# Performance work log

Measured on AMD Instinct MI355X. Metric: run time of the kernel, lower is better.

Reference implementation:

```python
import jax, jax.numpy as jnp
import numpy as np

B, C, H, W, K = 8, 128, 256, 256, 19


def setup_inputs() -> dict:
    key = jax.random.key(0)
    k1, k2, k3, k4, k5, k6 = jax.random.split(key, 6)
    s = 1.0 / np.sqrt(C)
    return {
        "x": jax.random.normal(k1, (B, C, H, W), dtype=jnp.float32),
        "preds": jax.random.normal(k2, (B, K, H, W), dtype=jnp.float32),
        "w1": jax.random.normal(k3, (C, C), dtype=jnp.float32) * s,
        "b1": jax.random.normal(k4, (C,), dtype=jnp.float32) * 0.01,
        "w2": jax.random.normal(k5, (C, C), dtype=jnp.float32) * s,
        "b2": jax.random.normal(k6, (C,), dtype=jnp.float32) * 0.01,
    }


def reference(x, preds, w1, b1, w2, b2):
    b, c, h, w = x.shape
    k = preds.shape[1]
    n = h * w
    xf = x.reshape(b, c, n)          # [B,C,N]
    pf = preds.reshape(b, k, n)      # [B,K,N]

    # --- GCG: argmax-grouped softmax-weighted segment sum, scatter back ---
    cls = jnp.argmax(pf, axis=1)                       # [B,N] per-pixel class
    m = jax.nn.one_hot(cls, k, axis=1, dtype=bool)     # [B,K,N] class membership
    scores = jnp.where(m, pf, -jnp.inf)                # mask logits per class group
    mx = jnp.max(scores, axis=2, keepdims=True)
    mx = jnp.where(jnp.isfinite(mx), mx, 0.0)          # guard empty classes
    e = jnp.where(m, jnp.exp(scores - mx), 0.0)
    wgt = e / jnp.maximum(e.sum(axis=2, keepdims=True), 1e-30)  # [B,K,N] segment softmax
    class_feats = jnp.einsum('bkn,bcn->bkc', wgt, xf)  # [B,K,C] weighted segment sum
    fs = jnp.take_along_axis(class_feats, cls[:, :, None], axis=1)  # [B,N,C] scatter-broadcast

    # --- 1x1 convs + global class attention ---
    x1 = jnp.einsum('bcn,dc->bdn', xf, w1) + b1[None, :, None]  # conv1 -> [B,C,N]
    fs2 = jnp.einsum('bnc,dc->bnd', fs, w2) + b2                # conv2 -> [B,N,C]
    gc = jnp.einsum('bcn,bnd->bcd', x1, fs2) * (c ** -0.5)      # [B,C,C]
    return jax.nn.softmax(gc, axis=-1)
```

## Files before the change

### kernel.cpp

```cpp
#include <hip/hip_runtime.h>

#define K_CLS 19
#define C_CH  128
#define NPIX  65536
#define BATCH 8
#define ROWSTRIDE 39


__global__ __launch_bounds__(256, 2)
void gcg_pass1(const float* __restrict__ preds, unsigned* __restrict__ meta,
               float* __restrict__ deng, float* __restrict__ cntg)
{
    __shared__ float denl[K_CLS], cntl[K_CLS];
    const int t = threadIdx.x;
    const int b = blockIdx.x >> 6, blk = blockIdx.x & 63;
    if (t < K_CLS) { denl[t] = 0.f; cntl[t] = 0.f; }
    __syncthreads();

    const int n0 = blk * 1024 + 4 * t;
    const float* pb = preds + (size_t)b * K_CLS * NPIX + n0;

    float4 bv = *reinterpret_cast<const float4*>(pb);
    int k0 = 0, k1 = 0, k2 = 0, k3 = 0;
    #pragma unroll
    for (int k = 1; k < K_CLS; ++k) {
        const float4 p = *reinterpret_cast<const float4*>(pb + (size_t)k * NPIX);
        if (p.x > bv.x) { bv.x = p.x; k0 = k; }
        if (p.y > bv.y) { bv.y = p.y; k1 = k; }
        if (p.z > bv.z) { bv.z = p.z; k2 = k; }
        if (p.w > bv.w) { bv.w = p.w; k3 = k; }
    }
    uint4 m;
    m.x = (__float_as_uint(__expf(bv.x)) & 0xFFFFFFE0u) | (unsigned)k0;
    m.y = (__float_as_uint(__expf(bv.y)) & 0xFFFFFFE0u) | (unsigned)k1;
    m.z = (__float_as_uint(__expf(bv.z)) & 0xFFFFFFE0u) | (unsigned)k2;
    m.w = (__float_as_uint(__expf(bv.w)) & 0xFFFFFFE0u) | (unsigned)k3;
    *reinterpret_cast<uint4*>(meta + (size_t)b * NPIX + n0) = m;

    atomicAdd(&denl[k0], __uint_as_float(m.x & 0xFFFFFFE0u)); atomicAdd(&cntl[k0], 1.f);
    atomicAdd(&denl[k1], __uint_as_float(m.y & 0xFFFFFFE0u)); atomicAdd(&cntl[k1], 1.f);
    atomicAdd(&denl[k2], __uint_as_float(m.z & 0xFFFFFFE0u)); atomicAdd(&cntl[k2], 1.f);
    atomicAdd(&denl[k3], __uint_as_float(m.w & 0xFFFFFFE0u)); atomicAdd(&cntl[k3], 1.f);
    __syncthreads();
    if (t < K_CLS) {
        unsafeAtomicAdd(&deng[b * K_CLS + t], denl[t]);
        unsafeAtomicAdd(&cntg[b * K_CLS + t], cntl[t]);
    }
}

__global__ __launch_bounds__(256, 4)
void gcg_pass2(const float* __restrict__ x, const unsigned* __restrict__ meta,
               float* __restrict__ WXg, float* __restrict__ SXg)
{
    __shared__ float acc[256 * ROWSTRIDE];
    const int t = threadIdx.x, w = t >> 6, l = t & 63;
    const int b = blockIdx.x >> 7;
    const int r = blockIdx.x & 127;
    const int cgrp = r >> 2, q = r & 3;
    const int c = cgrp * 4 + w;

    float* arow = &acc[t * ROWSTRIDE];
    #pragma unroll
    for (int s = 0; s < ROWSTRIDE; ++s) arow[s] = 0.f;

    const float*    xr = x    + ((size_t)(b * C_CH + c)) * NPIX + q * 16384;
    const unsigned* mr = meta + (size_t)b * NPIX + q * 16384;

    #pragma unroll 4
    for (int i = 0; i < 64; ++i) {
        const int px = i * 256 + 4 * l;
        const float4 x4 = *reinterpret_cast<const float4*>(xr + px);
        const uint4  m4 = *reinterpret_cast<const uint4*>(mr + px);
        {   const int k = (int)(m4.x & 31u);
            const float e = __uint_as_float(m4.x & 0xFFFFFFE0u);
            const float vW = arow[k], vS = arow[19 + k];
            arow[k] = fmaf(e, x4.x, vW); arow[19 + k] = vS + x4.x;
        }
        {   const int k = (int)(m4.y & 31u);
            const float e = __uint_as_float(m4.y & 0xFFFFFFE0u);
            const float vW = arow[k], vS = arow[19 + k];
            arow[k] = fmaf(e, x4.y, vW); arow[19 + k] = vS + x4.y;
        }
        {   const int k = (int)(m4.z & 31u);
            const float e = __uint_as_float(m4.z & 0xFFFFFFE0u);
            const float vW = arow[k], vS = arow[19 + k];
            arow[k] = fmaf(e, x4.z, vW); arow[19 + k] = vS + x4.z;
        }
        {   const int k = (int)(m4.w & 31u);
            const float e = __uint_as_float(m4.w & 0xFFFFFFE0u);
            const float vW = arow[k], vS = arow[19 + k];
            arow[k] = fmaf(e, x4.w, vW); arow[19 + k] = vS + x4.w;
        }
    }
    __syncthreads();

    if (t < 2 * 4 * K_CLS) {
        const int arr = t / (4 * K_CLS), rem = t % (4 * K_CLS);
        const int ww = rem / K_CLS, k = rem % K_CLS;
        const int slot = arr * K_CLS + k;
        float s0 = 0.f;
        #pragma unroll 8
        for (int ll = 0; ll < 64; ++ll)
            s0 += acc[(ww * 64 + ll) * ROWSTRIDE + slot];
        const int cc = cgrp * 4 + ww;
        float* dst = (arr == 0) ? WXg : SXg;
        unsafeAtomicAdd(&dst[((size_t)b * K_CLS + k) * C_CH + cc], s0);
    }
}

__global__ __launch_bounds__(256, 1)
void gcg_epiA(const float* __restrict__ WXg, const float* __restrict__ SXg,
              const float* __restrict__ deng, const float* __restrict__ cntg,
              const float* __restrict__ w1, const float* __restrict__ b1,
              const float* __restrict__ w2,
              float* __restrict__ cf2g, float* __restrict__ S1g)
{
    __shared__ float wb[C_CH * 129];
    __shared__ float fb[K_CLS * 129];
    const int t = threadIdx.x, b = blockIdx.x;

    for (int f = t; f < C_CH * C_CH / 4; f += 256) {
        const int d = f >> 5, c4 = (f & 31) << 2;
        const float4 v = *reinterpret_cast<const float4*>(w2 + d * C_CH + c4);
        float* p = &wb[d * 129 + c4];
        p[0] = v.x; p[1] = v.y; p[2] = v.z; p[3] = v.w;
    }
    for (int i = t; i < K_CLS * C_CH; i += 256) {
        const int k = i >> 7, c = i & 127;
        fb[k * 129 + c] = WXg[(size_t)b * K_CLS * C_CH + i] /
                          fmaxf(deng[b * K_CLS + k], 1e-30f);
    }
    __syncthreads();
    for (int i = t; i < K_CLS * C_CH; i += 256) {
        const int k = i >> 7, d = i & 127;
        float a = 0.f;
        #pragma unroll 8
        for (int c = 0; c < C_CH; ++c) a = fmaf(fb[k * 129 + c], wb[d * 129 + c], a);
        cf2g[(size_t)b * K_CLS * C_CH + k * C_CH + d] = a;
    }
    __syncthreads();
    for (int f = t; f < C_CH * C_CH / 4; f += 256) {
        const int d = f >> 5, c4 = (f & 31) << 2;
        const float4 v = *reinterpret_cast<const float4*>(w1 + d * C_CH + c4);
        float* p = &wb[d * 129 + c4];
        p[0] = v.x; p[1] = v.y; p[2] = v.z; p[3] = v.w;
    }
    for (int i = t; i < K_CLS * C_CH; i += 256)
        fb[(i >> 7) * 129 + (i & 127)] = SXg[(size_t)b * K_CLS * C_CH + i];
    __syncthreads();
    for (int i = t; i < K_CLS * C_CH; i += 256) {
        const int d = i / K_CLS, k = i % K_CLS;
        float a = 0.f;
        #pragma unroll 8
        for (int c = 0; c < C_CH; ++c) a = fmaf(wb[d * 129 + c], fb[k * 129 + c], a);
        S1g[(size_t)b * C_CH * K_CLS + d * K_CLS + k] = a + b1[d] * cntg[b * K_CLS + k];
    }
}

__global__ __launch_bounds__(256, 1)
void gcg_epiB(const float* __restrict__ cf2g, const float* __restrict__ S1g,
              const float* __restrict__ b2, float* __restrict__ out)
{
    __shared__ float cf2b[K_CLS * 132];
    __shared__ float S1b[16][20];
    __shared__ float b2b[C_CH];
    __shared__ float gcb[16][C_CH + 1];
    const int t = threadIdx.x;
    const int b = blockIdx.x >> 3, sl = blockIdx.x & 7;
    const int r0 = sl * 16;

    for (int i = t; i < K_CLS * C_CH; i += 256)
        cf2b[(i >> 7) * 132 + (i & 127)] = cf2g[(size_t)b * K_CLS * C_CH + i];
    for (int i = t; i < 16 * K_CLS; i += 256) {
        const int rr = i / K_CLS, k = i % K_CLS;
        S1b[rr][k] = S1g[(size_t)b * C_CH * K_CLS + (r0 + rr) * K_CLS + k];
    }
    if (t < C_CH) b2b[t] = b2[t];
    __syncthreads();

    {
        const int rr = t >> 4, d0 = (t & 15) * 8;
        float a0=0,a1=0,a2=0,a3=0,a4=0,a5=0,a6=0,a7=0, T = 0.f;
        #pragma unroll
        for (int k = 0; k < K_CLS; ++k) {
            const float sv = S1b[rr][k];
            T += sv;
            const float* row = &cf2b[k * 132 + d0];
            a0 = fmaf(sv, row[0], a0); a1 = fmaf(sv, row[1], a1);
            a2 = fmaf(sv, row[2], a2); a3 = fmaf(sv, row[3], a3);
            a4 = fmaf(sv, row[4], a4); a5 = fmaf(sv, row[5], a5);
            a6 = fmaf(sv, row[6], a6); a7 = fmaf(sv, row[7], a7);
        }
        const float s = 0.08838834764831845f;
        float* g = &gcb[rr][d0];
        g[0]=(a0+T*b2b[d0+0])*s; g[1]=(a1+T*b2b[d0+1])*s;
        g[2]=(a2+T*b2b[d0+2])*s; g[3]=(a3+T*b2b[d0+3])*s;
        g[4]=(a4+T*b2b[d0+4])*s; g[5]=(a5+T*b2b[d0+5])*s;
        g[6]=(a6+T*b2b[d0+6])*s; g[7]=(a7+T*b2b[d0+7])*s;
    }
    __syncthreads();

    const int wv = t >> 6, lane = t & 63;
    for (int rr = wv; rr < 16; rr += 4) {
        float v0 = gcb[rr][lane], v1 = gcb[rr][lane + 64];
        float m = fmaxf(v0, v1);
        #pragma unroll
        for (int o = 32; o > 0; o >>= 1) m = fmaxf(m, __shfl_xor(m, o));
        const float e0 = __expf(v0 - m), e1 = __expf(v1 - m);
        float ss = e0 + e1;
        #pragma unroll
        for (int o = 32; o > 0; o >>= 1) ss += __shfl_xor(ss, o);
        const float inv = 1.0f / ss;
        float* orow = out + ((size_t)b * C_CH + r0 + rr) * C_CH;
        orow[lane]      = e0 * inv;
        orow[lane + 64] = e1 * inv;
    }
}

extern "C" void kernel_launch(void* const* d_in, const int* in_sizes, int n_in,
                              void* d_out, int out_size, void* d_ws, size_t ws_size,
                              hipStream_t stream) {
    const float* x     = (const float*)d_in[0];
    const float* preds = (const float*)d_in[1];
    const float* w1    = (const float*)d_in[2];
    const float* b1    = (const float*)d_in[3];
    const float* w2    = (const float*)d_in[4];
    const float* b2    = (const float*)d_in[5];
    float* out = (float*)d_out;

    float* ws   = (float*)d_ws;
    float* WXg  = ws;
    float* SXg  = ws + 19456;
    float* deng = ws + 38912;
    float* cntg = ws + 39064;
    unsigned* META = (unsigned*)(ws + 39216);
    float* CF2  = ws + 563504;
    float* S1   = ws + 582960;

    hipMemsetAsync(d_ws, 0, 39216 * sizeof(float), stream);

    gcg_pass1<<<BATCH * 64, 256, 0, stream>>>(preds, META, deng, cntg);
    gcg_pass2<<<BATCH * 128, 256, 0, stream>>>(x, META, WXg, SXg);
    gcg_epiA<<<BATCH, 256, 0, stream>>>(WXg, SXg, deng, cntg, w1, b1, w2, CF2, S1);
    gcg_epiB<<<BATCH * 8, 256, 0, stream>>>(CF2, S1, b2, out);
}
```

Before: 445.3 us.

## Replace global atomics with per-block partials, drop memset, split epilogue A across two blocks per batch

```diff
diff --git a/kernel.cpp b/kernel.cpp
--- a/kernel.cpp
+++ b/kernel.cpp
@@ -4,12 +4,12 @@
 #define C_CH  128
 #define NPIX  65536
 #define BATCH 8
-#define ROWSTRIDE 39
+#define RS2   38
 
 
 __global__ __launch_bounds__(256, 2)
 void gcg_pass1(const float* __restrict__ preds, unsigned* __restrict__ meta,
-               float* __restrict__ deng, float* __restrict__ cntg)
+               float* __restrict__ denp)
 {
     __shared__ float denl[K_CLS], cntl[K_CLS];
     const int t = threadIdx.x;
@@ -43,25 +43,25 @@
     atomicAdd(&denl[k3], __uint_as_float(m.w & 0xFFFFFFE0u)); atomicAdd(&cntl[k3], 1.f);
     __syncthreads();
     if (t < K_CLS) {
-        unsafeAtomicAdd(&deng[b * K_CLS + t], denl[t]);
-        unsafeAtomicAdd(&cntg[b * K_CLS + t], cntl[t]);
+        denp[(size_t)blockIdx.x * RS2 + t]         = denl[t];
+        denp[(size_t)blockIdx.x * RS2 + K_CLS + t] = cntl[t];
     }
 }
 
 __global__ __launch_bounds__(256, 4)
 void gcg_pass2(const float* __restrict__ x, const unsigned* __restrict__ meta,
-               float* __restrict__ WXg, float* __restrict__ SXg)
-{
-    __shared__ float acc[256 * ROWSTRIDE];
+               float* __restrict__ part)
+{
+    __shared__ float acc[256 * RS2];
     const int t = threadIdx.x, w = t >> 6, l = t & 63;
     const int b = blockIdx.x >> 7;
     const int r = blockIdx.x & 127;
     const int cgrp = r >> 2, q = r & 3;
     const int c = cgrp * 4 + w;
 
-    float* arow = &acc[t * ROWSTRIDE];
+    float* arow = &acc[t * RS2];
     #pragma unroll
-    for (int s = 0; s < ROWSTRIDE; ++s) arow[s] = 0.f;
+    for (int s = 0; s < RS2; ++s) arow[s] = 0.f;
 
     const float*    xr = x    + ((size_t)(b * C_CH + c)) * NPIX + q * 16384;
     const unsigned* mr = meta + (size_t)b * NPIX + q * 16384;
@@ -73,23 +73,27 @@
         const uint4  m4 = *reinterpret_cast<const uint4*>(mr + px);
         {   const int k = (int)(m4.x & 31u);
             const float e = __uint_as_float(m4.x & 0xFFFFFFE0u);
-            const float vW = arow[k], vS = arow[19 + k];
-            arow[k] = fmaf(e, x4.x, vW); arow[19 + k] = vS + x4.x;
+            float2 v = *reinterpret_cast<float2*>(&arow[2 * k]);
+            v.x = fmaf(e, x4.x, v.x); v.y += x4.x;
+            *reinterpret_cast<float2*>(&arow[2 * k]) = v;
         }
         {   const int k = (int)(m4.y & 31u);
             const float e = __uint_as_float(m4.y & 0xFFFFFFE0u);
-            const float vW = arow[k], vS = arow[19 + k];
-            arow[k] = fmaf(e, x4.y, vW); arow[19 + k] = vS + x4.y;
+            float2 v = *reinterpret_cast<float2*>(&arow[2 * k]);
+            v.x = fmaf(e, x4.y, v.x); v.y += x4.y;
+            *reinterpret_cast<float2*>(&arow[2 * k]) = v;
         }
         {   const int k = (int)(m4.z & 31u);
             const float e = __uint_as_float(m4.z & 0xFFFFFFE0u);
-            const float vW = arow[k], vS = arow[19 + k];
-            arow[k] = fmaf(e, x4.z, vW); arow[19 + k] = vS + x4.z;
+            float2 v = *reinterpret_cast<float2*>(&arow[2 * k]);
+            v.x = fmaf(e, x4.z, v.x); v.y += x4.z;
+            *reinterpret_cast<float2*>(&arow[2 * k]) = v;
         }
         {   const int k = (int)(m4.w & 31u);
             const float e = __uint_as_float(m4.w & 0xFFFFFFE0u);
-            const float vW = arow[k], vS = arow[19 + k];
-            arow[k] = fmaf(e, x4.w, vW); arow[19 + k] = vS + x4.w;
+            float2 v = *reinterpret_cast<float2*>(&arow[2 * k]);
+            v.x = fmaf(e, x4.w, v.x); v.y += x4.w;
+            *reinterpret_cast<float2*>(&arow[2 * k]) = v;
         }
     }
     __syncthreads();
@@ -97,63 +101,67 @@
     if (t < 2 * 4 * K_CLS) {
         const int arr = t / (4 * K_CLS), rem = t % (4 * K_CLS);
         const int ww = rem / K_CLS, k = rem % K_CLS;
-        const int slot = arr * K_CLS + k;
         float s0 = 0.f;
         #pragma unroll 8
         for (int ll = 0; ll < 64; ++ll)
-            s0 += acc[(ww * 64 + ll) * ROWSTRIDE + slot];
-        const int cc = cgrp * 4 + ww;
-        float* dst = (arr == 0) ? WXg : SXg;
-        unsafeAtomicAdd(&dst[((size_t)b * K_CLS + k) * C_CH + cc], s0);
+            s0 += acc[(ww * 64 + ll) * RS2 + 2 * k + arr];
+        part[(size_t)blockIdx.x * 152 + arr * 76 + ww * K_CLS + k] = s0;
     }
 }
 
 __global__ __launch_bounds__(256, 1)
-void gcg_epiA(const float* __restrict__ WXg, const float* __restrict__ SXg,
-              const float* __restrict__ deng, const float* __restrict__ cntg,
+void gcg_epiA(const float* __restrict__ part, const float* __restrict__ denp,
               const float* __restrict__ w1, const float* __restrict__ b1,
               const float* __restrict__ w2,
               float* __restrict__ cf2g, float* __restrict__ S1g)
 {
     __shared__ float wb[C_CH * 129];
     __shared__ float fb[K_CLS * 129];
-    const int t = threadIdx.x, b = blockIdx.x;
-
+    __shared__ float redb[K_CLS];
+    const int t = threadIdx.x;
+    const int b = blockIdx.x >> 1, half = blockIdx.x & 1;
+
+    const float* wsrc = half ? w1 : w2;
     for (int f = t; f < C_CH * C_CH / 4; f += 256) {
         const int d = f >> 5, c4 = (f & 31) << 2;
-        const float4 v = *reinterpret_cast<const float4*>(w2 + d * C_CH + c4);
+        const float4 v = *reinterpret_cast<const float4*>(wsrc + d * C_CH + c4);
         float* p = &wb[d * 129 + c4];
         p[0] = v.x; p[1] = v.y; p[2] = v.z; p[3] = v.w;
     }
+    if (t < K_CLS) {
+        float s0 = 0.f;
+        const float* dp = denp + (size_t)(b * 64) * RS2 + half * K_CLS + t;
+        for (int blk = 0; blk < 64; ++blk) s0 += dp[(size_t)blk * RS2];
+        redb[t] = s0;
+    }
+    __syncthreads();
+
     for (int i = t; i < K_CLS * C_CH; i += 256) {
         const int k = i >> 7, c = i & 127;
-        fb[k * 129 + c] = WXg[(size_t)b * K_CLS * C_CH + i] /
-                          fmaxf(deng[b * K_CLS + k], 1e-30f);
-    }
-    __syncthreads();
-    for (int i = t; i < K_CLS * C_CH; i += 256) {
-        const int k = i >> 7, d = i & 127;
-        float a = 0.f;
-        #pragma unroll 8
-        for (int c = 0; c < C_CH; ++c) a = fmaf(fb[k * 129 + c], wb[d * 129 + c], a);
-        cf2g[(size_t)b * K_CLS * C_CH + k * C_CH + d] = a;
-    }
-    __syncthreads();
-    for (int f = t; f < C_CH * C_CH / 4; f += 256) {
-        const int d = f >> 5, c4 = (f & 31) << 2;
-        const float4 v = *reinterpret_cast<const float4*>(w1 + d * C_CH + c4);
-        float* p = &wb[d * 129 + c4];
-        p[0] = v.x; p[1] = v.y; p[2] = v.z; p[3] = v.w;
-    }
-    for (int i = t; i < K_CLS * C_CH; i += 256)
-        fb[(i >> 7) * 129 + (i & 127)] = SXg[(size_t)b * K_CLS * C_CH + i];
-    __syncthreads();
-    for (int i = t; i < K_CLS * C_CH; i += 256) {
-        const int d = i / K_CLS, k = i % K_CLS;
-        float a = 0.f;
-        #pragma unroll 8
-        for (int c = 0; c < C_CH; ++c) a = fmaf(wb[d * 129 + c], fb[k * 129 + c], a);
-        S1g[(size_t)b * C_CH * K_CLS + d * K_CLS + k] = a + b1[d] * cntg[b * K_CLS + k];
+        const int cgrp = c >> 2, ww = c & 3;
+        const float* pp = part + (size_t)(b * 128 + cgrp * 4) * 152 + half * 76 + ww * K_CLS + k;
+        float s0 = pp[0] + pp[152] + pp[304] + pp[456];
+        if (half == 0) s0 /= fmaxf(redb[k], 1e-30f);
+        fb[k * 129 + c] = s0;
+    }
+    __syncthreads();
+
+    if (half == 0) {
+        for (int i = t; i < K_CLS * C_CH; i += 256) {
+            const int k = i >> 7, d = i & 127;
+            float a = 0.f;
+            #pragma unroll 8
+            for (int c = 0; c < C_CH; ++c) a = fmaf(fb[k * 129 + c], wb[d * 129 + c], a);
+            cf2g[(size_t)b * K_CLS * C_CH + k * C_CH + d] = a;
+        }
+    } else {
+        for (int i = t; i < C_CH * K_CLS; i += 256) {
+            const int d = i / K_CLS, k = i % K_CLS;
+            float a = 0.f;
+            #pragma unroll 8
+            for (int c = 0; c < C_CH; ++c) a = fmaf(wb[d * 129 + c], fb[k * 129 + c], a);
+            S1g[(size_t)b * C_CH * K_CLS + d * K_CLS + k] = a + b1[d] * redb[k];
+        }
     }
 }
 
@@ -228,19 +236,15 @@
     const float* b2    = (const float*)d_in[5];
     float* out = (float*)d_out;
 
-    float* ws   = (float*)d_ws;
-    float* WXg  = ws;
-    float* SXg  = ws + 19456;
-    float* deng = ws + 38912;
-    float* cntg = ws + 39064;
-    unsigned* META = (unsigned*)(ws + 39216);
-    float* CF2  = ws + 563504;
-    float* S1   = ws + 582960;
-
-    hipMemsetAsync(d_ws, 0, 39216 * sizeof(float), stream);
-
-    gcg_pass1<<<BATCH * 64, 256, 0, stream>>>(preds, META, deng, cntg);
-    gcg_pass2<<<BATCH * 128, 256, 0, stream>>>(x, META, WXg, SXg);
-    gcg_epiA<<<BATCH, 256, 0, stream>>>(WXg, SXg, deng, cntg, w1, b1, w2, CF2, S1);
+    float* ws      = (float*)d_ws;
+    unsigned* META = (unsigned*)ws;
+    float* PART = ws + 524288;
+    float* DENP = ws + 679936;
+    float* CF2  = ws + 699392;
+    float* S1   = ws + 718848;
+
+    gcg_pass1<<<BATCH * 64, 256, 0, stream>>>(preds, META, DENP);
+    gcg_pass2<<<BATCH * 128, 256, 0, stream>>>(x, META, PART);
+    gcg_epiA<<<BATCH * 2, 256, 0, stream>>>(PART, DENP, w1, b1, w2, CF2, S1);
     gcg_epiB<<<BATCH * 8, 256, 0, stream>>>(CF2, S1, b2, out);
 }
```

Result: faster. 430.3 us (-3.3%).
